# Kernel optimization log

Hardware: AMD Instinct MI355X
Metric: run time of the kernel (lower is better)

## Reference

```python
import jax, jax.numpy as jnp
import numpy as np

N_NODES = 100000
F_IN = 512
HIDDEN = 64
N_CLASS = 40
N_EDGES = 3200000


def gcn_conv(x, src, dst, deg_inv_sqrt, W, b, n_nodes):
    # PyG GCNConv: linear transform, then deg^{-1/2} A_hat deg^{-1/2} aggregation, then bias
    h = x @ W  # [N, out]
    norm = deg_inv_sqrt[src] * deg_inv_sqrt[dst]  # [E+N] (includes self-loops)
    msg = h[src] * norm[:, None]  # gather + scale
    out = jax.ops.segment_sum(msg, dst, num_segments=n_nodes)  # scatter-add
    return out + b


def setup_inputs() -> dict:
    key = jax.random.key(0)
    k1, k2, k3, k4, k5 = jax.random.split(key, 5)
    x = jax.random.normal(k1, (N_NODES, F_IN), dtype=jnp.float32)
    edge_index = jax.random.randint(k2, (2, N_EDGES), 0, N_NODES, dtype=jnp.int64)
    # Glorot-style init for GCN weights
    W1 = jax.random.normal(k3, (F_IN, HIDDEN), dtype=jnp.float32) / np.sqrt(F_IN)
    b1 = jnp.zeros((HIDDEN,), dtype=jnp.float32)
    W2 = jax.random.normal(k4, (HIDDEN, N_CLASS), dtype=jnp.float32) / np.sqrt(HIDDEN)
    b2 = jnp.zeros((N_CLASS,), dtype=jnp.float32)
    return {"x": x, "edge_index": edge_index, "W1": W1, "b1": b1, "W2": W2, "b2": b2}


def reference(x, edge_index, W1, b1, W2, b2):
    n = x.shape[0]
    loops = jnp.arange(n, dtype=edge_index.dtype)
    src = jnp.concatenate([edge_index[0], loops])  # add self-loops (GCNConv default)
    dst = jnp.concatenate([edge_index[1], loops])
    deg = jax.ops.segment_sum(jnp.ones_like(dst, dtype=x.dtype), dst, num_segments=n)
    deg_inv_sqrt = jnp.where(deg > 0, jax.lax.rsqrt(deg), 0.0)
    h = gcn_conv(x, src, dst, deg_inv_sqrt, W1, b1, n)
    h = jax.nn.relu(h)  # dropout treated as eval-mode identity
    x_out = gcn_conv(h, src, dst, deg_inv_sqrt, W2, b2, n)
    return jax.nn.log_softmax(x_out, axis=1), x_out
```

## Files before the change

### kernel.cpp

```cpp
#include <hip/hip_runtime.h>
#include <math.h>

#define N_NODES 100000
#define F_IN    512
#define HIDDEN  64
#define N_CLASS 40
#define N_EDGES 3200000
#define NB      782
#define CAP     6144
#define EPB     8192
#define NPB     391

typedef int EIdx;

typedef __attribute__((ext_vector_type(8))) short short8;
typedef __attribute__((ext_vector_type(4))) float f32x4;
typedef __attribute__((ext_vector_type(4))) unsigned uint4v;

__device__ inline short f2bf(float f) {
    unsigned u = __builtin_bit_cast(unsigned, f);
    unsigned r = u + 0x7FFFu + ((u >> 16) & 1u);
    return (short)(r >> 16);
}

__device__ inline unsigned cvtpk(float lo, float hi) {
    unsigned r;
    asm("v_cvt_pk_bf16_f32 %0, %1, %2" : "=v"(r) : "v"(lo), "v"(hi));
    return r;
}

__device__ inline float bflo(unsigned w) { return __builtin_bit_cast(float, w << 16); }
__device__ inline float bfhi(unsigned w) { return __builtin_bit_cast(float, w & 0xFFFF0000u); }

__global__ __launch_bounds__(256) void wprep_kernel(const float* __restrict__ W,
                                                    short* __restrict__ Wbf,
                                                    int* __restrict__ bcur) {
    int idx = blockIdx.x * 256 + threadIdx.x;
    if (idx < NB) bcur[idx] = idx * CAP;
    int k = idx >> 6, col = idx & 63;
    Wbf[col * F_IN + (k ^ ((col & 7) << 3))] = f2bf(W[idx]);
}

__global__ __launch_bounds__(256) void part1_kernel(const EIdx* __restrict__ src,
                                                    const EIdx* __restrict__ dst,
                                                    int* __restrict__ bcur,
                                                    unsigned* __restrict__ bpacked) {
    __shared__ int hist[2 * NB];
    __shared__ int excl[NB];
    __shared__ int cur[2 * NB];
    __shared__ int delta[NB];
    __shared__ int stmp[256];
    __shared__ unsigned spk[EPB];
    __shared__ unsigned short bid[EPB];
    int t = threadIdx.x;
    int sub = t >> 7;
    int e0 = blockIdx.x * EPB;
    int dreg[32];
    for (int j = t; j < 2 * NB; j += 256) hist[j] = 0;
    __syncthreads();
#pragma unroll
    for (int k = 0; k < 32; ++k) {
        int e = e0 + k * 256 + t;
        dreg[k] = (e < N_EDGES) ? dst[e] : -1;
        if (dreg[k] >= 0) atomicAdd(&hist[sub * NB + (dreg[k] >> 7)], 1);
    }
    __syncthreads();
    {
        int i0 = 4 * t;
        int v0 = (i0 < NB) ? hist[i0] + hist[NB + i0] : 0;
        int v1 = (i0 + 1 < NB) ? hist[i0 + 1] + hist[NB + i0 + 1] : 0;
        int v2 = (i0 + 2 < NB) ? hist[i0 + 2] + hist[NB + i0 + 2] : 0;
        int v3 = (i0 + 3 < NB) ? hist[i0 + 3] + hist[NB + i0 + 3] : 0;
        int s = v0 + v1 + v2 + v3;
        stmp[t] = s;
        __syncthreads();
        for (int o = 1; o < 256; o <<= 1) {
            int a = (t >= o) ? stmp[t - o] : 0;
            __syncthreads();
            stmp[t] += a;
            __syncthreads();
        }
        int E = stmp[t] - s;
        if (i0 < NB) excl[i0] = E;
        if (i0 + 1 < NB) excl[i0 + 1] = E + v0;
        if (i0 + 2 < NB) excl[i0 + 2] = E + v0 + v1;
        if (i0 + 3 < NB) excl[i0 + 3] = E + v0 + v1 + v2;
    }
    __syncthreads();
    for (int j = t; j < NB; j += 256) {
        int h0 = hist[j], h1 = hist[NB + j];
        int tot = h0 + h1;
        int rsv = tot ? atomicAdd(&bcur[j], tot) : 0;
        delta[j] = rsv - excl[j];
        cur[j] = excl[j];
        cur[NB + j] = excl[j] + h0;
    }
    __syncthreads();
#pragma unroll
    for (int k = 0; k < 32; ++k) {
        int d = dreg[k];
        if (d >= 0) {
            int e = e0 + k * 256 + t;
            int s = src[e];
            int b = d >> 7;
            int p = atomicAdd(&cur[sub * NB + b], 1);
            spk[p] = ((unsigned)(d & 127) << 20) | (unsigned)s;
            bid[p] = (unsigned short)b;
        }
    }
    __syncthreads();
    int cnt = N_EDGES - e0;
    if (cnt > EPB) cnt = EPB;
    for (int i = t; i < cnt; i += 256) {
        int bb = bid[i];
        int pos = i + delta[bb];
        if (pos < (bb + 1) * CAP) bpacked[pos] = spk[i];
    }
}

__global__ __launch_bounds__(256) void part2_kernel(const int* __restrict__ bcur,
                                                    const unsigned* __restrict__ bpacked,
                                                    int* __restrict__ csr_src,
                                                    unsigned* __restrict__ rowmeta,
                                                    float* __restrict__ dis) {
    __shared__ unsigned ent[CAP];
    __shared__ int hist[2 * 128];
    __shared__ int stmp[128];
    __shared__ int cur[2 * 128];
    int t = threadIdx.x;
    int sub = t >> 7;
    int bk = blockIdx.x;
    int base = bk * CAP;
    int cnt = bcur[bk] - base;
    if (cnt > CAP) cnt = CAP;
    hist[t] = 0;
    __syncthreads();
    for (int i = t; i < cnt; i += 256) {
        unsigned p = bpacked[base + i];
        ent[i] = p;
        atomicAdd(&hist[sub * 128 + (p >> 20)], 1);
    }
    __syncthreads();
    if (t < 128) stmp[t] = hist[t] + hist[128 + t];
    __syncthreads();
    for (int o = 1; o < 128; o <<= 1) {
        int a = (t >= o && t < 128) ? stmp[t - o] : 0;
        __syncthreads();
        if (t < 128) stmp[t] += a;
        __syncthreads();
    }
    if (t < 128) {
        int tot = hist[t] + hist[128 + t];
        int ex = stmp[t] - tot;
        cur[t] = ex;
        cur[128 + t] = ex + hist[t];
        int n = (bk << 7) + t;
        if (n < N_NODES) {
            rowmeta[n] = (unsigned)(base + ex) | ((unsigned)tot << 23);
            dis[n] = rsqrtf((float)(tot + 1));
        }
    }
    __syncthreads();
    for (int i = t; i < cnt; i += 256) {
        unsigned p = ent[i];
        int p2 = atomicAdd(&cur[sub * 128 + (p >> 20)], 1);
        csr_src[base + p2] = (int)(p & 0xFFFFFu);
    }
}

__global__ __launch_bounds__(256) void gemm1_mfma_kernel(const float* __restrict__ x,
                                                         const short* __restrict__ Wbf,
                                                         const float* __restrict__ dis,
                                                         unsigned* __restrict__ h1b) {
    __shared__ short Wt[HIDDEN * 128];
    __shared__ short xs[128 * 72];
    int tid = threadIdx.x;
    int wave = tid >> 6, lane = tid & 63;
    int r0 = blockIdx.x * 128;
    int wr0 = r0 + wave * 32;
    int lrow = lane & 15;
    int lk = (lane >> 4) * 8;
    int bswz = (lane & 7) << 3;

    f32x4 acc[2][4];
#pragma unroll
    for (int m = 0; m < 2; ++m)
#pragma unroll
        for (int n = 0; n < 4; ++n) acc[m][n] = (f32x4)0.0f;

    int srow = tid >> 4;
    int schunk = tid & 15;
    int grow[8];
#pragma unroll
    for (int i = 0; i < 8; ++i) {
        int r = r0 + srow + i * 16;
        grow[i] = (r < N_NODES) ? r : (N_NODES - 1);
    }

    float4 xr[8];
#pragma unroll
    for (int i = 0; i < 8; ++i)
        xr[i] = *reinterpret_cast<const float4*>(x + (size_t)grow[i] * F_IN + 4 * schunk);

    const short8* Wv = (const short8*)Wbf;
    short8* Lv = (short8*)Wt;

    for (int ks = 0; ks < 8; ++ks) {
        int kg = ks * 64;
        __syncthreads();
#pragma unroll
        for (int i = 0; i < 8; ++i) {
            uint2 u = {cvtpk(xr[i].x, xr[i].y), cvtpk(xr[i].z, xr[i].w)};
            *reinterpret_cast<uint2*>(&xs[(srow + i * 16) * 72 + 4 * schunk]) = u;
        }
        if ((ks & 1) == 0) {
            int q = ks >> 1;
            for (int i = tid; i < 1024; i += 256) {
                int col = i >> 4, kc = i & 15;
                Lv[i] = Wv[col * 64 + q * 16 + kc];
            }
        }
        __syncthreads();
        if (ks < 7) {
            int kn = kg + 64;
#pragma unroll
            for (int i = 0; i < 8; ++i)
                xr[i] = *reinterpret_cast<const float4*>(x + (size_t)grow[i] * F_IN + kn + 4 * schunk);
        }
#pragma unroll
        for (int s = 0; s < 2; ++s) {
            int kwq = (ks & 1) * 64 + s * 32;
            int kloc = s * 32;
            short8 a0 = *reinterpret_cast<const short8*>(&xs[(wave * 32 + lrow) * 72 + kloc + lk]);
            short8 a1 = *reinterpret_cast<const short8*>(&xs[(wave * 32 + 16 + lrow) * 72 + kloc + lk]);
            short8 b[4];
#pragma unroll
            for (int n = 0; n < 4; ++n) {
                int c = n * 16 + lrow;
                b[n] = *reinterpret_cast<const short8*>(&Wt[c * 128 + ((kwq + lk) ^ bswz)]);
            }
#pragma unroll
            for (int n = 0; n < 4; ++n) {
                acc[0][n] = __builtin_amdgcn_mfma_f32_16x16x32_bf16(a0, b[n], acc[0][n], 0, 0, 0);
                acc[1][n] = __builtin_amdgcn_mfma_f32_16x16x32_bf16(a1, b[n], acc[1][n], 0, 0, 0);
            }
        }
    }

    int crow = (lane >> 4) * 4, ccol = lane & 15;
    bool evenc = (ccol & 1) == 0;
#pragma unroll
    for (int m = 0; m < 2; ++m) {
#pragma unroll
        for (int j = 0; j < 4; ++j) {
            int rr = wr0 + m * 16 + crow + j;
            int rs = (rr < N_NODES) ? rr : (N_NODES - 1);
            float ds = dis[rs];
            float v[4], vn[4];
#pragma unroll
            for (int n = 0; n < 4; ++n) v[n] = acc[m][n][j] * ds;
#pragma unroll
            for (int n = 0; n < 4; ++n) vn[n] = __shfl_xor(v[n], 1);
            if (rr < N_NODES && evenc) {
#pragma unroll
                for (int n = 0; n < 4; ++n)
                    h1b[(size_t)rr * 32 + ((n * 16 + ccol) >> 1)] = cvtpk(v[n], vn[n]);
            }
        }
    }
}

__global__ __launch_bounds__(256) void gather1_gemm2_kernel(const unsigned* __restrict__ h1b,
                                                            const unsigned* __restrict__ rowmeta,
                                                            const int* __restrict__ csr_src,
                                                            const float* __restrict__ dis,
                                                            const float* __restrict__ b1,
                                                            const float* __restrict__ W2,
                                                            unsigned* __restrict__ h2b) {
    __shared__ float W2s[HIDDEN * N_CLASS];
    __shared__ float aggs[32 * HIDDEN];
    __shared__ float outs[32 * N_CLASS];
    int tid = threadIdx.x;
    for (int i = tid; i < HIDDEN * N_CLASS; i += 256) W2s[i] = W2[i];

    int nl = tid >> 3;
    int n = blockIdx.x * 32 + nl;
    int l = tid & 7;
    unsigned meta = rowmeta[n];
    int base = (int)(meta & 0x7FFFFFu);
    int deg = (int)(meta >> 23);
    const unsigned* rowp = h1b + 4 * l;
    uint4 v = *reinterpret_cast<const uint4*>(h1b + (size_t)n * 32 + 4 * l);
    float a0 = bflo(v.x), a1 = bfhi(v.x), a2 = bflo(v.y), a3 = bfhi(v.y);
    float a4 = bflo(v.z), a5 = bfhi(v.z), a6 = bflo(v.w), a7 = bfhi(v.w);
    int e = 0;
    for (; e + 7 < deg; e += 8) {
        int s0 = csr_src[base + e],     s1 = csr_src[base + e + 1];
        int s2 = csr_src[base + e + 2], s3 = csr_src[base + e + 3];
        int s4 = csr_src[base + e + 4], s5 = csr_src[base + e + 5];
        int s6 = csr_src[base + e + 6], s7 = csr_src[base + e + 7];
        uint4 r0 = *reinterpret_cast<const uint4*>(rowp + (size_t)s0 * 32);
        uint4 r1 = *reinterpret_cast<const uint4*>(rowp + (size_t)s1 * 32);
        uint4 r2 = *reinterpret_cast<const uint4*>(rowp + (size_t)s2 * 32);
        uint4 r3 = *reinterpret_cast<const uint4*>(rowp + (size_t)s3 * 32);
        uint4 r4 = *reinterpret_cast<const uint4*>(rowp + (size_t)s4 * 32);
        uint4 r5 = *reinterpret_cast<const uint4*>(rowp + (size_t)s5 * 32);
        uint4 r6 = *reinterpret_cast<const uint4*>(rowp + (size_t)s6 * 32);
        uint4 r7 = *reinterpret_cast<const uint4*>(rowp + (size_t)s7 * 32);
        a0 += ((bflo(r0.x) + bflo(r1.x)) + (bflo(r2.x) + bflo(r3.x))) +
              ((bflo(r4.x) + bflo(r5.x)) + (bflo(r6.x) + bflo(r7.x)));
        a1 += ((bfhi(r0.x) + bfhi(r1.x)) + (bfhi(r2.x) + bfhi(r3.x))) +
              ((bfhi(r4.x) + bfhi(r5.x)) + (bfhi(r6.x) + bfhi(r7.x)));
        a2 += ((bflo(r0.y) + bflo(r1.y)) + (bflo(r2.y) + bflo(r3.y))) +
              ((bflo(r4.y) + bflo(r5.y)) + (bflo(r6.y) + bflo(r7.y)));
        a3 += ((bfhi(r0.y) + bfhi(r1.y)) + (bfhi(r2.y) + bfhi(r3.y))) +
              ((bfhi(r4.y) + bfhi(r5.y)) + (bfhi(r6.y) + bfhi(r7.y)));
        a4 += ((bflo(r0.z) + bflo(r1.z)) + (bflo(r2.z) + bflo(r3.z))) +
              ((bflo(r4.z) + bflo(r5.z)) + (bflo(r6.z) + bflo(r7.z)));
        a5 += ((bfhi(r0.z) + bfhi(r1.z)) + (bfhi(r2.z) + bfhi(r3.z))) +
              ((bfhi(r4.z) + bfhi(r5.z)) + (bfhi(r6.z) + bfhi(r7.z)));
        a6 += ((bflo(r0.w) + bflo(r1.w)) + (bflo(r2.w) + bflo(r3.w))) +
              ((bflo(r4.w) + bflo(r5.w)) + (bflo(r6.w) + bflo(r7.w)));
        a7 += ((bfhi(r0.w) + bfhi(r1.w)) + (bfhi(r2.w) + bfhi(r3.w))) +
              ((bfhi(r4.w) + bfhi(r5.w)) + (bfhi(r6.w) + bfhi(r7.w)));
    }
    for (; e < deg; ++e) {
        int s = csr_src[base + e];
        uint4 r = *reinterpret_cast<const uint4*>(rowp + (size_t)s * 32);
        a0 += bflo(r.x); a1 += bfhi(r.x); a2 += bflo(r.y); a3 += bfhi(r.y);
        a4 += bflo(r.z); a5 += bfhi(r.z); a6 += bflo(r.w); a7 += bfhi(r.w);
    }
    float ds = dis[n];
    {
        float4 bL = *reinterpret_cast<const float4*>(b1 + 8 * l);
        float4 bH = *reinterpret_cast<const float4*>(b1 + 8 * l + 4);
        float4 oL = {fmaxf(fmaf(a0, ds, bL.x), 0.f), fmaxf(fmaf(a1, ds, bL.y), 0.f),
                     fmaxf(fmaf(a2, ds, bL.z), 0.f), fmaxf(fmaf(a3, ds, bL.w), 0.f)};
        float4 oH = {fmaxf(fmaf(a4, ds, bH.x), 0.f), fmaxf(fmaf(a5, ds, bH.y), 0.f),
                     fmaxf(fmaf(a6, ds, bH.z), 0.f), fmaxf(fmaf(a7, ds, bH.w), 0.f)};
        float* ap = aggs + nl * HIDDEN + 8 * l;
        *reinterpret_cast<float4*>(ap) = oL;
        *reinterpret_cast<float4*>(ap + 4) = oH;
    }
    __syncthreads();
    {
        float o0 = 0.f, o1 = 0.f, o2 = 0.f, o3 = 0.f, o4 = 0.f;
        const float* ar = aggs + nl * HIDDEN;
        int c0 = 5 * l;
#pragma unroll 8
        for (int k = 0; k < HIDDEN; ++k) {
            float av = ar[k];
            const float* wr = W2s + k * N_CLASS + c0;
            o0 = fmaf(av, wr[0], o0);
            o1 = fmaf(av, wr[1], o1);
            o2 = fmaf(av, wr[2], o2);
            o3 = fmaf(av, wr[3], o3);
            o4 = fmaf(av, wr[4], o4);
        }
        float* op = outs + nl * N_CLASS + c0;
        op[0] = o0 * ds; op[1] = o1 * ds; op[2] = o2 * ds; op[3] = o3 * ds; op[4] = o4 * ds;
    }
    __syncthreads();
    for (int i = tid; i < 32 * 20; i += 256) {
        int n3 = i / 20, c3 = i % 20;
        const float* op = outs + n3 * N_CLASS + 2 * c3;
        h2b[(size_t)(blockIdx.x * 32 + n3) * 20 + c3] = cvtpk(op[0], op[1]);
    }
}

__global__ __launch_bounds__(256) void gather2_kernel(const unsigned* __restrict__ h2b,
                                                      const unsigned* __restrict__ rowmeta,
                                                      const int* __restrict__ csr_src,
                                                      const float* __restrict__ dis,
                                                      const float* __restrict__ b2,
                                                      float* __restrict__ xout,
                                                      float* __restrict__ out_ls) {
    int tid = threadIdx.x;
    int n = blockIdx.x * 32 + (tid >> 3);
    int l = tid & 7;
    bool act = l < 5;
    unsigned meta = rowmeta[n];
    int base = (int)(meta & 0x7FFFFFu);
    int deg = (int)(meta >> 23);
    const unsigned* rowp = h2b + 4 * l;
    float a0 = 0.f, a1 = 0.f, a2 = 0.f, a3 = 0.f, a4 = 0.f, a5 = 0.f, a6 = 0.f, a7 = 0.f;
    if (act) {
        uint4 v = *reinterpret_cast<const uint4*>(h2b + (size_t)n * 20 + 4 * l);
        a0 = bflo(v.x); a1 = bfhi(v.x); a2 = bflo(v.y); a3 = bfhi(v.y);
        a4 = bflo(v.z); a5 = bfhi(v.z); a6 = bflo(v.w); a7 = bfhi(v.w);
    }
    int e = 0;
    for (; e + 7 < deg; e += 8) {
        int s0 = csr_src[base + e],     s1 = csr_src[base + e + 1];
        int s2 = csr_src[base + e + 2], s3 = csr_src[base + e + 3];
        int s4 = csr_src[base + e + 4], s5 = csr_src[base + e + 5];
        int s6 = csr_src[base + e + 6], s7 = csr_src[base + e + 7];
        if (act) {
            uint4 r0 = *reinterpret_cast<const uint4*>(rowp + (size_t)s0 * 20);
            uint4 r1 = *reinterpret_cast<const uint4*>(rowp + (size_t)s1 * 20);
            uint4 r2 = *reinterpret_cast<const uint4*>(rowp + (size_t)s2 * 20);
            uint4 r3 = *reinterpret_cast<const uint4*>(rowp + (size_t)s3 * 20);
            uint4 r4 = *reinterpret_cast<const uint4*>(rowp + (size_t)s4 * 20);
            uint4 r5 = *reinterpret_cast<const uint4*>(rowp + (size_t)s5 * 20);
            uint4 r6 = *reinterpret_cast<const uint4*>(rowp + (size_t)s6 * 20);
            uint4 r7 = *reinterpret_cast<const uint4*>(rowp + (size_t)s7 * 20);
            a0 += ((bflo(r0.x) + bflo(r1.x)) + (bflo(r2.x) + bflo(r3.x))) +
                  ((bflo(r4.x) + bflo(r5.x)) + (bflo(r6.x) + bflo(r7.x)));
            a1 += ((bfhi(r0.x) + bfhi(r1.x)) + (bfhi(r2.x) + bfhi(r3.x))) +
                  ((bfhi(r4.x) + bfhi(r5.x)) + (bfhi(r6.x) + bfhi(r7.x)));
            a2 += ((bflo(r0.y) + bflo(r1.y)) + (bflo(r2.y) + bflo(r3.y))) +
                  ((bflo(r4.y) + bflo(r5.y)) + (bflo(r6.y) + bflo(r7.y)));
            a3 += ((bfhi(r0.y) + bfhi(r1.y)) + (bfhi(r2.y) + bfhi(r3.y))) +
                  ((bfhi(r4.y) + bfhi(r5.y)) + (bfhi(r6.y) + bfhi(r7.y)));
            a4 += ((bflo(r0.z) + bflo(r1.z)) + (bflo(r2.z) + bflo(r3.z))) +
                  ((bflo(r4.z) + bflo(r5.z)) + (bflo(r6.z) + bflo(r7.z)));
            a5 += ((bfhi(r0.z) + bfhi(r1.z)) + (bfhi(r2.z) + bfhi(r3.z))) +
                  ((bfhi(r4.z) + bfhi(r5.z)) + (bfhi(r6.z) + bfhi(r7.z)));
            a6 += ((bflo(r0.w) + bflo(r1.w)) + (bflo(r2.w) + bflo(r3.w))) +
                  ((bflo(r4.w) + bflo(r5.w)) + (bflo(r6.w) + bflo(r7.w)));
            a7 += ((bfhi(r0.w) + bfhi(r1.w)) + (bfhi(r2.w) + bfhi(r3.w))) +
                  ((bfhi(r4.w) + bfhi(r5.w)) + (bfhi(r6.w) + bfhi(r7.w)));
        }
    }
    for (; e < deg; ++e) {
        int s = csr_src[base + e];
        if (act) {
            uint4 r = *reinterpret_cast<const uint4*>(rowp + (size_t)s * 20);
            a0 += bflo(r.x); a1 += bfhi(r.x); a2 += bflo(r.y); a3 += bfhi(r.y);
            a4 += bflo(r.z); a5 += bfhi(r.z); a6 += bflo(r.w); a7 += bfhi(r.w);
        }
    }
    float ds = dis[n];
    float v0 = 0.f, v1 = 0.f, v2 = 0.f, v3 = 0.f, v4 = 0.f, v5 = 0.f, v6 = 0.f, v7 = 0.f;
    if (act) {
        float4 bL = *reinterpret_cast<const float4*>(b2 + 8 * l);
        float4 bH = *reinterpret_cast<const float4*>(b2 + 8 * l + 4);
        v0 = fmaf(a0, ds, bL.x); v1 = fmaf(a1, ds, bL.y);
        v2 = fmaf(a2, ds, bL.z); v3 = fmaf(a3, ds, bL.w);
        v4 = fmaf(a4, ds, bH.x); v5 = fmaf(a5, ds, bH.y);
        v6 = fmaf(a6, ds, bH.z); v7 = fmaf(a7, ds, bH.w);
    }
    float mx = act ? fmaxf(fmaxf(fmaxf(v0, v1), fmaxf(v2, v3)),
                           fmaxf(fmaxf(v4, v5), fmaxf(v6, v7))) : -INFINITY;
    mx = fmaxf(mx, __shfl_xor(mx, 1));
    mx = fmaxf(mx, __shfl_xor(mx, 2));
    mx = fmaxf(mx, __shfl_xor(mx, 4));
    float sum = act ? ((expf(v0 - mx) + expf(v1 - mx)) + (expf(v2 - mx) + expf(v3 - mx))) +
                      ((expf(v4 - mx) + expf(v5 - mx)) + (expf(v6 - mx) + expf(v7 - mx))) : 0.f;
    sum += __shfl_xor(sum, 1);
    sum += __shfl_xor(sum, 2);
    sum += __shfl_xor(sum, 4);
    if (act) {
        float ls = mx + logf(sum);
        float* xp = xout + (size_t)n * N_CLASS + 8 * l;
        float* lp = out_ls + (size_t)n * N_CLASS + 8 * l;
        float4 xoL = {v0, v1, v2, v3};
        float4 xoH = {v4, v5, v6, v7};
        float4 loL = {v0 - ls, v1 - ls, v2 - ls, v3 - ls};
        float4 loH = {v4 - ls, v5 - ls, v6 - ls, v7 - ls};
        *reinterpret_cast<float4*>(xp) = xoL;
        *reinterpret_cast<float4*>(xp + 4) = xoH;
        *reinterpret_cast<float4*>(lp) = loL;
        *reinterpret_cast<float4*>(lp + 4) = loH;
    }
}

extern "C" void kernel_launch(void* const* d_in, const int* in_sizes, int n_in,
                              void* d_out, int out_size, void* d_ws, size_t ws_size,
                              hipStream_t stream) {
    const float* x  = (const float*)d_in[0];
    const EIdx*  ei = (const EIdx*)d_in[1];
    const float* W1 = (const float*)d_in[2];
    const float* b1 = (const float*)d_in[3];
    const float* W2 = (const float*)d_in[4];
    const float* b2 = (const float*)d_in[5];
    const EIdx* src = ei;
    const EIdx* dst = ei + N_EDGES;

    float* out_ls = (float*)d_out;
    float* x_out  = out_ls + (size_t)N_NODES * N_CLASS;

    char* w = (char*)d_ws;
    int*      bcur    = (int*)w;       w += 1024 * 4;
    float*    dis     = (float*)w;     w += 100352 * 4;
    unsigned* rowmeta = (unsigned*)w;  w += 100352 * 4;
    short*    Wbf     = (short*)w;     w += (size_t)F_IN * HIDDEN * 2;
    unsigned* bpacked = (unsigned*)w;
    unsigned* h1b     = (unsigned*)w;  w += (size_t)NB * CAP * 4;
    int*      csr_src = (int*)w;       w += (size_t)NB * CAP * 4;
    unsigned* h2b     = (unsigned*)w;  w += (size_t)N_NODES * 20 * 4;

    const int B = 256;
    int gG  = N_NODES / 32;
    int gM1 = (N_NODES + 127) / 128;

    wprep_kernel<<<(F_IN * HIDDEN) / B, B, 0, stream>>>(W1, Wbf, bcur);
    part1_kernel<<<NPB, B, 0, stream>>>(src, dst, bcur, bpacked);
    part2_kernel<<<NB, B, 0, stream>>>(bcur, bpacked, csr_src, rowmeta, dis);

    gemm1_mfma_kernel<<<gM1, B, 0, stream>>>(x, Wbf, dis, h1b);
    gather1_gemm2_kernel<<<gG, B, 0, stream>>>(h1b, rowmeta, csr_src, dis, b1, W2, h2b);

    gather2_kernel<<<gG, B, 0, stream>>>(h2b, rowmeta, csr_src, dis, b2, x_out, out_ls);
}
```

Before: 263.4 us.

## Fuse CSR bucket sort with first GEMM into one kernel sharing LDS

Merges the per-bucket CSR construction (part2) and the bf16 MFMA x@W1 GEMM into a single kernel, since both use 128-node blocks (NB equals the GEMM grid). The first x loads are issued before the sort so that their latency overlaps it, and the degree normalisation is read from LDS instead of global memory. LDS is reused through one aliased buffer. h1b no longer aliases bpacked, so the workspace grows. The sort's synchronisation now sits in front of the GEMM, and the larger LDS and register footprint may lower occupancy.

```diff
diff --git a/kernel.cpp b/kernel.cpp
--- a/kernel.cpp
+++ b/kernel.cpp
@@ -118,65 +118,83 @@
     }
 }
 
-__global__ __launch_bounds__(256) void part2_kernel(const int* __restrict__ bcur,
-                                                    const unsigned* __restrict__ bpacked,
-                                                    int* __restrict__ csr_src,
-                                                    unsigned* __restrict__ rowmeta,
-                                                    float* __restrict__ dis) {
-    __shared__ unsigned ent[CAP];
-    __shared__ int hist[2 * 128];
-    __shared__ int stmp[128];
-    __shared__ int cur[2 * 128];
+__global__ __launch_bounds__(256) void part2_gemm1_kernel(const int* __restrict__ bcur,
+                                                          const unsigned* __restrict__ bpacked,
+                                                          const float* __restrict__ x,
+                                                          const short* __restrict__ Wbf,
+                                                          int* __restrict__ csr_src,
+                                                          unsigned* __restrict__ rowmeta,
+                                                          float* __restrict__ dis,
+                                                          unsigned* __restrict__ h1b) {
+    __shared__ __align__(16) char smem[34816];
+    __shared__ float disL[128];
+    unsigned* ent = (unsigned*)smem;
+    int* hist = (int*)(smem + 24576);
+    int* stmp = (int*)(smem + 25600);
+    int* cur  = (int*)(smem + 26112);
+    short* Wt = (short*)smem;
+    short* xs = (short*)(smem + 16384);
+
     int t = threadIdx.x;
-    int sub = t >> 7;
     int bk = blockIdx.x;
-    int base = bk * CAP;
-    int cnt = bcur[bk] - base;
-    if (cnt > CAP) cnt = CAP;
-    hist[t] = 0;
-    __syncthreads();
-    for (int i = t; i < cnt; i += 256) {
-        unsigned p = bpacked[base + i];
-        ent[i] = p;
-        atomicAdd(&hist[sub * 128 + (p >> 20)], 1);
-    }
-    __syncthreads();
-    if (t < 128) stmp[t] = hist[t] + hist[128 + t];
-    __syncthreads();
-    for (int o = 1; o < 128; o <<= 1) {
-        int a = (t >= o && t < 128) ? stmp[t - o] : 0;
-        __syncthreads();
-        if (t < 128) stmp[t] += a;
-        __syncthreads();
-    }
-    if (t < 128) {
-        int tot = hist[t] + hist[128 + t];
-        int ex = stmp[t] - tot;
-        cur[t] = ex;
-        cur[128 + t] = ex + hist[t];
-        int n = (bk << 7) + t;
-        if (n < N_NODES) {
-            rowmeta[n] = (unsigned)(base + ex) | ((unsigned)tot << 23);
-            dis[n] = rsqrtf((float)(tot + 1));
-        }
-    }
-    __syncthreads();
-    for (int i = t; i < cnt; i += 256) {
-        unsigned p = ent[i];
-        int p2 = atomicAdd(&cur[sub * 128 + (p >> 20)], 1);
-        csr_src[base + p2] = (int)(p & 0xFFFFFu);
-    }
-}
-
-__global__ __launch_bounds__(256) void gemm1_mfma_kernel(const float* __restrict__ x,
-                                                         const short* __restrict__ Wbf,
-                                                         const float* __restrict__ dis,
-                                                         unsigned* __restrict__ h1b) {
-    __shared__ short Wt[HIDDEN * 128];
-    __shared__ short xs[128 * 72];
-    int tid = threadIdx.x;
-    int wave = tid >> 6, lane = tid & 63;
-    int r0 = blockIdx.x * 128;
+    int r0 = bk << 7;
+
+    int srow = t >> 4;
+    int schunk = t & 15;
+    int grow[8];
+#pragma unroll
+    for (int i = 0; i < 8; ++i) {
+        int r = r0 + srow + i * 16;
+        grow[i] = (r < N_NODES) ? r : (N_NODES - 1);
+    }
+    float4 xr[8];
+#pragma unroll
+    for (int i = 0; i < 8; ++i)
+        xr[i] = *reinterpret_cast<const float4*>(x + (size_t)grow[i] * F_IN + 4 * schunk);
+
+    {
+        int sub = t >> 7;
+        int base = bk * CAP;
+        int cnt = bcur[bk] - base;
+        if (cnt > CAP) cnt = CAP;
+        hist[t] = 0;
+        __syncthreads();
+        for (int i = t; i < cnt; i += 256) {
+            unsigned p = bpacked[base + i];
+            ent[i] = p;
+            atomicAdd(&hist[sub * 128 + (p >> 20)], 1);
+        }
+        __syncthreads();
+        if (t < 128) stmp[t] = hist[t] + hist[128 + t];
+        __syncthreads();
+        for (int o = 1; o < 128; o <<= 1) {
+            int a = (t >= o && t < 128) ? stmp[t - o] : 0;
+            __syncthreads();
+            if (t < 128) stmp[t] += a;
+            __syncthreads();
+        }
+        if (t < 128) {
+            int tot = hist[t] + hist[128 + t];
+            int ex = stmp[t] - tot;
+            cur[t] = ex;
+            cur[128 + t] = ex + hist[t];
+            float dsv = rsqrtf((float)(tot + 1));
+            disL[t] = dsv;
+            int n = r0 + t;
+            if (n < N_NODES) {
+                rowmeta[n] = (unsigned)(base + ex) | ((unsigned)tot << 23);
+                dis[n] = dsv;
+            }
+        }
+        __syncthreads();
+        for (int i = t; i < cnt; i += 256) {
+            unsigned p = ent[i];
+            int p2 = atomicAdd(&cur[sub * 128 + (p >> 20)], 1);
+            csr_src[base + p2] = (int)(p & 0xFFFFFu);
+        }
+    }
+
+    int wave = t >> 6, lane = t & 63;
     int wr0 = r0 + wave * 32;
     int lrow = lane & 15;
     int lk = (lane >> 4) * 8;
@@ -188,20 +206,6 @@
 #pragma unroll
         for (int n = 0; n < 4; ++n) acc[m][n] = (f32x4)0.0f;
 
-    int srow = tid >> 4;
-    int schunk = tid & 15;
-    int grow[8];
-#pragma unroll
-    for (int i = 0; i < 8; ++i) {
-        int r = r0 + srow + i * 16;
-        grow[i] = (r < N_NODES) ? r : (N_NODES - 1);
-    }
-
-    float4 xr[8];
-#pragma unroll
-    for (int i = 0; i < 8; ++i)
-        xr[i] = *reinterpret_cast<const float4*>(x + (size_t)grow[i] * F_IN + 4 * schunk);
-
     const short8* Wv = (const short8*)Wbf;
     short8* Lv = (short8*)Wt;
 
@@ -215,7 +219,7 @@
         }
         if ((ks & 1) == 0) {
             int q = ks >> 1;
-            for (int i = tid; i < 1024; i += 256) {
+            for (int i = t; i < 1024; i += 256) {
                 int col = i >> 4, kc = i & 15;
                 Lv[i] = Wv[col * 64 + q * 16 + kc];
             }
@@ -255,7 +259,7 @@
         for (int j = 0; j < 4; ++j) {
             int rr = wr0 + m * 16 + crow + j;
             int rs = (rr < N_NODES) ? rr : (N_NODES - 1);
-            float ds = dis[rs];
+            float ds = disL[rs - r0];
             float v[4], vn[4];
 #pragma unroll
             for (int n = 0; n < 4; ++n) v[n] = acc[m][n][j] * ds;
@@ -485,20 +489,20 @@
     float*    dis     = (float*)w;     w += 100352 * 4;
     unsigned* rowmeta = (unsigned*)w;  w += 100352 * 4;
     short*    Wbf     = (short*)w;     w += (size_t)F_IN * HIDDEN * 2;
-    unsigned* bpacked = (unsigned*)w;
-    unsigned* h1b     = (unsigned*)w;  w += (size_t)NB * CAP * 4;
+    unsigned* bpacked = (unsigned*)w;  w += (size_t)NB * CAP * 4;
     int*      csr_src = (int*)w;       w += (size_t)NB * CAP * 4;
+    unsigned* h1b     = (unsigned*)w;  w += (size_t)N_NODES * 32 * 4;
     unsigned* h2b     = (unsigned*)w;  w += (size_t)N_NODES * 20 * 4;
 
     const int B = 256;
     int gG  = N_NODES / 32;
-    int gM1 = (N_NODES + 127) / 128;
 
     wprep_kernel<<<(F_IN * HIDDEN) / B, B, 0, stream>>>(W1, Wbf, bcur);
     part1_kernel<<<NPB, B, 0, stream>>>(src, dst, bcur, bpacked);
-    part2_kernel<<<NB, B, 0, stream>>>(bcur, bpacked, csr_src, rowmeta, dis);
-
-    gemm1_mfma_kernel<<<gM1, B, 0, stream>>>(x, Wbf, dis, h1b);
+
+    part2_gemm1_kernel<<<NB, B, 0, stream>>>(bcur, bpacked, x, Wbf,
+                                             csr_src, rowmeta, dis, h1b);
+
     gather1_gemm2_kernel<<<gG, B, 0, stream>>>(h1b, rowmeta, csr_src, dis, b1, W2, h2b);
 
     gather2_kernel<<<gG, B, 0, stream>>>(h2b, rowmeta, csr_src, dis, b2, x_out, out_ls);
```

Measured after the change: 264.2 us. No clear change (+0.3%).
